# Kernel tuning notes

Measured on AMD Instinct MI355X. Metric: run time of the kernel, lower is better.

## Reference

```python
import jax, jax.numpy as jnp
import numpy as np

B, T, M, E, H = 8, 1024, 8192, 1024, 128
DECAY = 0.01
LQ_ADD = 1e-4
POS_TABLE_SIZE = 32


def setup_inputs() -> dict:
    key = jax.random.key(0)
    ks = jax.random.split(key, 9)
    return {
        "block_pos_list": jax.random.randint(ks[0], (B,), 0, 10),
        "inp": jax.random.normal(ks[1], (B, T, E), jnp.float32),
        "memory": jax.random.normal(ks[2], (B, M, E), jnp.float32),
        "memory_block_dist": jax.random.randint(ks[3], (B, M), 0, 1000).astype(jnp.int32),
        "memory_rank": jax.random.normal(ks[4], (B, M), jnp.float32),
        "pos_table": jax.random.normal(ks[5], (POS_TABLE_SIZE, E), jnp.float32) * 0.02,
        "Wk": jax.random.normal(ks[6], (H, E), jnp.float32) / np.float32(np.sqrt(E)),
        "Wq": jax.random.normal(ks[7], (H, E), jnp.float32) / np.float32(np.sqrt(E)),
        "Wv": jax.random.normal(ks[8], (H, E), jnp.float32) / np.float32(np.sqrt(E)),
    }


def reference(block_pos_list, inp, memory, memory_block_dist, memory_rank, pos_table, Wk, Wq, Wv):
    # --- reset slots where block_pos == 0 (start of a new work) ---
    reset = (block_pos_list == 0)                               # [B]
    memory = jnp.where(reset[:, None, None], 0.0, memory)       # [B, M, E]
    dist = jnp.where(reset[:, None], 0, memory_block_dist) + 1  # [B, M]

    # --- log2-bucketed positional embedding added to memory ---
    m_pos_ix = jnp.floor(jnp.log2(dist.astype(jnp.float32))).astype(jnp.int32)
    m_with_emb = memory + pos_table[m_pos_ix]                   # [B, M, E]
    mk = jnp.concatenate([m_with_emb, inp], axis=1)             # [B, M+T, E]

    # --- projections (torch Linear: x @ W.T) ---
    k = jnp.einsum('bse,he->bsh', mk, Wk)                       # [B, M+T, H]
    q = jnp.einsum('bte,he->bth', inp, Wq)                      # [B, T, H]
    v = jnp.einsum('bse,he->bsh', mk, Wv)                       # [B, M+T, H]

    # --- square + max-normalize attention (not softmax) ---
    mbs = M + T
    wei = jnp.einsum('bth,bsh->bts', q, k) * np.float32(mbs ** -0.5)  # [B, T, M+T]
    wei = wei * wei
    wei = wei / jnp.max(wei, axis=2, keepdims=True)

    # --- per-slot rank update ---
    mean_wei = jnp.mean(jnp.sum(wei, axis=1), axis=1)           # [B]
    new_rank = memory_rank + jnp.sum(wei[:, :, :M], axis=1) / mean_wei[:, None] - 1.0 - DECAY

    # --- sort memory slots by rank (descending), evict bottom block ---
    order = jnp.argsort(-new_rank, axis=1)                      # [B, M]
    mem_s = jnp.take_along_axis(memory, order[:, :, None], axis=1)
    dist_s = jnp.take_along_axis(dist, order, axis=1)
    rank_s = jnp.take_along_axis(new_rank, order, axis=1)
    r = min(T, M)
    new_memory = jax.lax.stop_gradient(mem_s.at[:, -r:].set(inp[:, -r:]))
    new_dist = dist_s.at[:, -r:].set(0)
    new_rank_out = jax.lax.stop_gradient(rank_s.at[:, -r:].set(1.0))

    qt_loss = jnp.sum(jnp.log(wei + LQ_ADD))
    out = jnp.einsum('bts,bsh->bth', wei, v)                    # [B, T, H]
    return out, qt_loss, new_memory, new_dist, new_rank_out
```

## Files before the change

### kernel.cpp

```cpp
#include <hip/hip_runtime.h>
#include <hip/hip_bf16.h>
#include <stdint.h>

#define BB 8
#define TT 1024
#define MM 8192
#define EE 1024
#define HH 128
#define SS (MM + TT)
#define RKEEP (MM - 1024)
#define NSPLIT 4
#define SCHUNK (SS / NSPLIT)
#define NT (SCHUNK / 64)
#define BK 32
#define NKVBLK (SS / 64)

typedef __attribute__((ext_vector_type(8))) short bf16x8;
typedef __attribute__((ext_vector_type(4))) short s16x4;
typedef __attribute__((ext_vector_type(4))) float f32x4;

#define SBAR()   __builtin_amdgcn_s_barrier()
#define SCB()    __builtin_amdgcn_sched_barrier(0)

static __device__ __forceinline__ unsigned f2ord(float f) {
    unsigned u = __float_as_uint(f);
    return u ^ ((u & 0x80000000u) ? 0xFFFFFFFFu : 0x80000000u);
}
static __device__ __forceinline__ float ord2f(unsigned o) {
    unsigned u = (o & 0x80000000u) ? (o ^ 0x80000000u) : ~o;
    return __uint_as_float(u);
}
static __device__ __forceinline__ unsigned short f2bf(float x) {
    unsigned u = __float_as_uint(x);
    unsigned r = u + 0x7FFFu + ((u >> 16) & 1u);
    return (unsigned short)(r >> 16);
}

static __device__ __forceinline__ void gload_lds16(const short* g, short* l) {
    __builtin_amdgcn_global_load_lds(
        (const __attribute__((address_space(1))) void*)g,
        (__attribute__((address_space(3))) void*)l, 16, 0, 0);
}

__device__ const float SCALEF = (float)(1.0 / 96.0);

__global__ __launch_bounds__(256) void k_init(
    const float* __restrict__ Wk, const float* __restrict__ Wq, const float* __restrict__ Wv,
    short* __restrict__ wk, short* __restrict__ wq, short* __restrict__ wv,
    float* __restrict__ outZ, float* __restrict__ rmax)
{
    const int blk = blockIdx.x, tid = threadIdx.x;
    if (blk < 384) {
        int idx = blk * 256 + tid;
        int m = idx >> 15;
        int o4 = (idx & 32767) * 4;
        const float* W = m == 0 ? Wk : (m == 1 ? Wq : Wv);
        short* D = m == 0 ? wk : (m == 1 ? wq : wv);
        f32x4 v = *(const f32x4*)&W[o4];
        s16x4 h;
#pragma unroll
        for (int j = 0; j < 4; ++j) h[j] = (short)f2bf(v[j]);
        *(s16x4*)&D[o4] = h;
    } else {
        const int z = (blk - 384) * 256 + tid;
        const f32x4 zero = (f32x4){0.f, 0.f, 0.f, 0.f};
        for (int i = z; i < (BB * TT * HH) / 4; i += 128 * 256)
            ((f32x4*)outZ)[i] = zero;
        if (z == 0) outZ[BB * TT * HH] = 0.f;
        if (z < (BB * TT) / 4) ((f32x4*)rmax)[z] = zero;
    }
}

__global__ __launch_bounds__(256, 3) void k_proj(
    const float* __restrict__ memory, const int* __restrict__ mbd,
    const int* __restrict__ bpl, const float* __restrict__ pos_table,
    const float* __restrict__ inp,
    const short* __restrict__ wk, const short* __restrict__ wv,
    const short* __restrict__ wq,
    short* __restrict__ kb, short* __restrict__ vT, short* __restrict__ qb)
{
    __shared__ __align__(16) short smA[2][64 * 64];
    __shared__ __align__(16) short smB[2][2][128 * 32];

    const int tid = threadIdx.x;
    const int b   = blockIdx.y;
    const int lane = tid & 63, wid = tid >> 6;
    const int wc = wid;
    const int fr = lane & 15, fq = lane >> 4;
    const int arow = tid >> 2;
    const int aq   = tid & 3;
    const int wh   = (tid >> 2);
    const int wk8  = (tid & 3) * 8;
    const int wdst = wid * 512;

    if (blockIdx.x < NKVBLK) {
        const int s0 = blockIdx.x * 64;
        const bool reset = (bpl[b] == 0);
        int pix;
        const float* abase;
        {
            int s = s0 + arow;
            if (s < MM) {
                int d = reset ? 1 : (mbd[b * MM + s] + 1);
                pix = 31 - __clz(d);
                abase = reset ? nullptr : &memory[((size_t)b * MM + s) * EE];
            } else {
                pix = -1;
                abase = &inp[((size_t)b * TT + (s - MM)) * EE];
            }
        }

        f32x4 accK[4][2], accV[4][2];
#pragma unroll
        for (int m = 0; m < 4; ++m)
#pragma unroll
            for (int n = 0; n < 2; ++n) {
                accK[m][n] = (f32x4){0.f, 0.f, 0.f, 0.f};
                accV[m][n] = (f32x4){0.f, 0.f, 0.f, 0.f};
            }

        auto STAGEW = [&](int e0, int buf) {
#pragma unroll
            for (int p = 0; p < 2; ++p) {
                int h = p * 64 + wh;
                int ec = wk8 ^ ((h & 3) << 3);
                size_t g = (size_t)h * EE + e0 + ec;
                gload_lds16(&wk[g], &smB[buf][0][p * 2048 + wdst]);
                gload_lds16(&wv[g], &smB[buf][1][p * 2048 + wdst]);
            }
        };
        auto LOADP = [&](int p, f32x4 xa[4]) {
            int e0 = p * 64 + aq * 16;
#pragma unroll
            for (int j = 0; j < 4; ++j) {
                f32x4 v = (f32x4){0.f, 0.f, 0.f, 0.f};
                if (abase) v = *(const f32x4*)&abase[e0 + j * 4];
                if (pix >= 0) {
                    f32x4 pt = *(const f32x4*)&pos_table[(size_t)pix * EE + e0 + j * 4];
                    v[0] += pt[0]; v[1] += pt[1]; v[2] += pt[2]; v[3] += pt[3];
                }
                xa[j] = v;
            }
        };
        auto STOREP = [&](const f32x4 xa[4], int abuf) {
#pragma unroll
            for (int j = 0; j < 2; ++j) {
                bf16x8 h;
#pragma unroll
                for (int c = 0; c < 4; ++c) {
                    h[c]     = (short)f2bf(xa[2 * j][c]);
                    h[4 + c] = (short)f2bf(xa[2 * j + 1][c]);
                }
                int g = (aq * 2 + j) ^ (arow & 7);
                *(bf16x8*)&smA[abuf][arow * 64 + g * 8] = h;
            }
        };

        f32x4 xa[4];
        LOADP(0, xa);
        STOREP(xa, 0);
        STAGEW(0, 0);
        __syncthreads();
        LOADP(1, xa);

        for (int step = 0; step < 32; ++step) {
            const int wbuf = step & 1;
            const int sseg = step & 1;
            const int pbuf = (step >> 1) & 1;
            if (step < 31) STAGEW((step + 1) * BK, wbuf ^ 1);

            bf16x8 ah[4];
#pragma unroll
            for (int m = 0; m < 4; ++m) {
                int r = m * 16 + fr;
                int g = (sseg * 4 + fq) ^ (r & 7);
                ah[m] = *(const bf16x8*)&smA[pbuf][r * 64 + g * 8];
            }
#pragma unroll
            for (int n = 0; n < 2; ++n) {
                int c = wc * 32 + n * 16 + fr;
                int off = c * 32 + ((fq * 8) ^ ((c & 3) << 3));
                bf16x8 kh = *(const bf16x8*)&smB[wbuf][0][off];
                bf16x8 vh = *(const bf16x8*)&smB[wbuf][1][off];
#pragma unroll
                for (int m = 0; m < 4; ++m) {
                    accK[m][n] = __builtin_amdgcn_mfma_f32_16x16x32_bf16(ah[m], kh, accK[m][n], 0, 0, 0);
                    accV[m][n] = __builtin_amdgcn_mfma_f32_16x16x32_bf16(ah[m], vh, accV[m][n], 0, 0, 0);
                }
            }
            if (sseg == 1 && step < 31) STOREP(xa, pbuf ^ 1);
            __syncthreads();
            if (sseg == 1 && step < 29) LOADP((step >> 1) + 2, xa);
        }

#pragma unroll
        for (int m = 0; m < 4; ++m) {
            int row = s0 + m * 16 + fq * 4;
#pragma unroll
            for (int n = 0; n < 2; ++n) {
                int col = wc * 32 + n * 16 + fr;
#pragma unroll
                for (int i = 0; i < 4; ++i)
                    kb[((size_t)b * SS + row + i) * HH + col] = (short)f2bf(accK[m][n][i]);
            }
        }
        float* tpT = (float*)smB;
#pragma unroll
        for (int hp = 0; hp < 4; ++hp) {
            __syncthreads();
            if (wc == hp) {
#pragma unroll
                for (int m = 0; m < 4; ++m)
#pragma unroll
                    for (int n = 0; n < 2; ++n) {
                        int cl = n * 16 + fr;
                        int row = m * 16 + fq * 4;
                        *(f32x4*)&tpT[cl * 68 + row] = accV[m][n];
                    }
            }
            __syncthreads();
            for (int idx = tid; idx < 32 * 16; idx += 256) {
                int hcl = idx >> 4, s4 = (idx & 15) << 2;
                f32x4 v = *(const f32x4*)&tpT[hcl * 68 + s4];
                s16x4 hi;
#pragma unroll
                for (int j = 0; j < 4; ++j) hi[j] = (short)f2bf(v[j]);
                size_t o = ((size_t)b * HH + hp * 32 + hcl) * SS + s0 + s4;
                *(s16x4*)&vT[o] = hi;
            }
        }
    } else {
        const int t0 = (blockIdx.x - NKVBLK) * 64;
        const float* abase = &inp[((size_t)b * TT + t0 + arow) * EE];

        f32x4 acc[4][2];
#pragma unroll
        for (int m = 0; m < 4; ++m)
#pragma unroll
            for (int n = 0; n < 2; ++n) acc[m][n] = (f32x4){0.f, 0.f, 0.f, 0.f};

        auto STAGEWQ = [&](int e0, int buf) {
#pragma unroll
            for (int p = 0; p < 2; ++p) {
                int h = p * 64 + wh;
                int ec = wk8 ^ ((h & 3) << 3);
                size_t g = (size_t)h * EE + e0 + ec;
                gload_lds16(&wq[g], &smB[buf][0][p * 2048 + wdst]);
            }
        };
        auto LOADPQ = [&](int p, f32x4 xa[4]) {
            int e0 = p * 64 + aq * 16;
#pragma unroll
            for (int j = 0; j < 4; ++j) xa[j] = *(const f32x4*)&abase[e0 + j * 4];
        };
        auto STOREPQ = [&](const f32x4 xa[4], int abuf) {
#pragma unroll
            for (int j = 0; j < 2; ++j) {
                bf16x8 h;
#pragma unroll
                for (int c = 0; c < 4; ++c) {
                    h[c]     = (short)f2bf(xa[2 * j][c]);
                    h[4 + c] = (short)f2bf(xa[2 * j + 1][c]);
                }
                int g = (aq * 2 + j) ^ (arow & 7);
                *(bf16x8*)&smA[abuf][arow * 64 + g * 8] = h;
            }
        };

        f32x4 xa[4];
        LOADPQ(0, xa);
        STOREPQ(xa, 0);
        STAGEWQ(0, 0);
        __syncthreads();
        LOADPQ(1, xa);

        for (int step = 0; step < 32; ++step) {
            const int wbuf = step & 1;
            const int sseg = step & 1;
            const int pbuf = (step >> 1) & 1;
            if (step < 31) STAGEWQ((step + 1) * BK, wbuf ^ 1);

            bf16x8 ah[4];
#pragma unroll
            for (int m = 0; m < 4; ++m) {
                int r = m * 16 + fr;
                int g = (sseg * 4 + fq) ^ (r & 7);
                ah[m] = *(const bf16x8*)&smA[pbuf][r * 64 + g * 8];
            }
#pragma unroll
            for (int n = 0; n < 2; ++n) {
                int c = wc * 32 + n * 16 + fr;
                int off = c * 32 + ((fq * 8) ^ ((c & 3) << 3));
                bf16x8 bh = *(const bf16x8*)&smB[wbuf][0][off];
#pragma unroll
                for (int m = 0; m < 4; ++m)
                    acc[m][n] = __builtin_amdgcn_mfma_f32_16x16x32_bf16(ah[m], bh, acc[m][n], 0, 0, 0);
            }
            if (sseg == 1 && step < 31) STOREPQ(xa, pbuf ^ 1);
            __syncthreads();
            if (sseg == 1 && step < 29) LOADPQ((step >> 1) + 2, xa);
        }
#pragma unroll
        for (int m = 0; m < 4; ++m) {
            int row = t0 + m * 16 + fq * 4;
#pragma unroll
            for (int n = 0; n < 2; ++n) {
                int col = wc * 32 + n * 16 + fr;
#pragma unroll
                for (int i = 0; i < 4; ++i)
                    qb[((size_t)b * TT + row + i) * HH + col] = (short)f2bf(acc[m][n][i]);
            }
        }
    }
}

__device__ __forceinline__ void stage_k64_async(const short* __restrict__ src,
                                                size_t rowBase, int tid, short* sh)
{
#pragma unroll
    for (int c2 = 0; c2 < 4; ++c2) {
        int srow = c2 * 16 + (tid >> 4);
        int scol = ((tid & 15) * 8) ^ ((srow & 7) << 3);
        size_t g = (rowBase + srow) * HH + scol;
        gload_lds16(&src[g], &sh[c2 * 2048 + (tid >> 6) * 512]);
    }
}

__device__ __forceinline__ void stage_v64_async(const short* __restrict__ vT,
                                                int b, int st, int tid, short* vs)
{
#pragma unroll
    for (int c2 = 0; c2 < 4; ++c2) {
        int h = c2 * 32 + (tid >> 3);
        int sc = ((tid & 7) * 8) ^ ((h & 7) << 3);
        size_t g = ((size_t)b * HH + h) * SS + st + sc;
        gload_lds16(&vT[g], &vs[c2 * 2048 + (tid >> 6) * 512]);
    }
}

__device__ __forceinline__ void load_qfrags(const short* __restrict__ qb,
                                            size_t rowIx, int fq, bf16x8 qh[4])
{
    size_t base = rowIx * HH + fq * 8;
#pragma unroll
    for (int k = 0; k < 4; ++k)
        qh[k] = *(const bf16x8*)&qb[base + k * 32];
}

__device__ __forceinline__ void qk_mfma4(const bf16x8 qh[4], const short* sh,
                                         int fr, int fq, f32x4 acc[4])
{
#pragma unroll
    for (int n = 0; n < 4; ++n) {
        int sc = n * 16 + fr;
        int ro = sc * 128, msk = (sc & 7) << 3;
#pragma unroll
        for (int k = 0; k < 4; ++k) {
            int off = ro + ((k * 32 + fq * 8) ^ msk);
            bf16x8 bh = *(const bf16x8*)&sh[off];
            acc[n] = __builtin_amdgcn_mfma_f32_16x16x32_bf16(qh[k], bh, acc[n], 0, 0, 0);
        }
    }
}

__device__ __forceinline__ void xcd_remap(int f, int& b, int& split, int& ttile)
{
    int xcd = f & 7, slot = f >> 3;
    int g = (slot >> 4) * 8 + xcd;
    ttile = slot & 15;
    b = g >> 2;
    split = g & 3;
}

__global__ __launch_bounds__(256) void k_rowmax(
    const short* __restrict__ qb, const short* __restrict__ kb,
    float* __restrict__ rowmax)
{
    __shared__ short Ks[2][64 * 128];
    const int tid = threadIdx.x, lane = tid & 63, wloc = tid >> 6;
    const int fr = lane & 15, fq = lane >> 4;
    int b, split, ttile;
    xcd_remap(blockIdx.x, b, split, ttile);
    const int t0 = ttile * 64;

    bf16x8 qh[4];
    load_qfrags(qb, (size_t)b * TT + t0 + wloc * 16 + fr, fq, qh);

    float rm[4] = {0.f, 0.f, 0.f, 0.f};
    const int sBeg = split * SCHUNK;
    const size_t kbase = (size_t)b * SS;

    stage_k64_async(kb, kbase + sBeg, tid, Ks[0]);
    __syncthreads();
    for (int t = 0; t < NT; ++t) {
        const int bf = t & 1;
        if (t + 1 < NT)
            stage_k64_async(kb, kbase + sBeg + (t + 1) * 64, tid, Ks[bf ^ 1]);
        f32x4 acc[4];
#pragma unroll
        for (int n = 0; n < 4; ++n) acc[n] = (f32x4){0.f, 0.f, 0.f, 0.f};
        __builtin_amdgcn_s_setprio(1);
        qk_mfma4(qh, Ks[bf], fr, fq, acc);
        __builtin_amdgcn_s_setprio(0);
#pragma unroll
        for (int n = 0; n < 4; ++n)
#pragma unroll
            for (int i = 0; i < 4; ++i) {
                float w = acc[n][i] * SCALEF;
                rm[i] = fmaxf(rm[i], w * w);
            }
        __syncthreads();
    }
#pragma unroll
    for (int d = 1; d < 16; d <<= 1)
#pragma unroll
        for (int i = 0; i < 4; ++i)
            rm[i] = fmaxf(rm[i], __shfl_xor(rm[i], d, 64));
    if (fr == 0)
#pragma unroll
        for (int i = 0; i < 4; ++i)
            atomicMax((int*)&rowmax[b * TT + t0 + wloc * 16 + fq * 4 + i], __float_as_int(rm[i]));
}

__global__ __launch_bounds__(256) void k_attn(
    const short* __restrict__ qb, const short* __restrict__ kb,
    const short* __restrict__ vT,
    const float* __restrict__ rowmax,
    float* __restrict__ outAcc, float* __restrict__ cpart, float* __restrict__ qtloss)
{
    __shared__ short Ks[2][64 * 128];
    __shared__ short Vs[2][128 * 64];
    __shared__ short Ph[64 * 64];
    __shared__ float csT[2][64];
    __shared__ float qred[256];
    const int tid = threadIdx.x, lane = tid & 63, wloc = tid >> 6;
    const int fr = lane & 15, fq = lane >> 4;
    int b, split, ttile;
    xcd_remap(blockIdx.x, b, split, ttile);
    const int t0 = ttile * 64;

    if (tid < 128) ((float*)csT)[tid] = 0.f;

    bf16x8 qh[4];
    load_qfrags(qb, (size_t)b * TT + t0 + wloc * 16 + fr, fq, qh);

    float inv[4];
#pragma unroll
    for (int i = 0; i < 4; ++i)
        inv[i] = 1.0f / rowmax[b * TT + t0 + wloc * 16 + fq * 4 + i];

    f32x4 oacc[8];
#pragma unroll
    for (int n = 0; n < 8; ++n) oacc[n] = (f32x4){0.f, 0.f, 0.f, 0.f};
    float qtp = 0.f;

    const int sBeg = split * SCHUNK;
    const size_t kbase = (size_t)b * SS;
    float* cprow = &cpart[((size_t)(b * 16 + ttile)) * SS + sBeg];

    stage_k64_async(kb, kbase + sBeg, tid, Ks[0]);
    stage_v64_async(vT, b, sBeg, tid, Vs[0]);

    for (int t = 0; t < NT; ++t) {
        const int bf = t & 1;
        __syncthreads();

        if (t + 1 < NT) {
            stage_k64_async(kb, kbase + sBeg + (t + 1) * 64, tid, Ks[bf ^ 1]);
            stage_v64_async(vT, b, sBeg + (t + 1) * 64, tid, Vs[bf ^ 1]);
        }

        f32x4 acc[4];
#pragma unroll
        for (int n = 0; n < 4; ++n) acc[n] = (f32x4){0.f, 0.f, 0.f, 0.f};
        __builtin_amdgcn_s_setprio(1);
        qk_mfma4(qh, Ks[bf], fr, fq, acc);
        __builtin_amdgcn_s_setprio(0);

        float prod = 1.f;
#pragma unroll
        for (int n = 0; n < 4; ++n) {
            float cp = 0.f;
#pragma unroll
            for (int i = 0; i < 4; ++i) {
                float w = acc[n][i] * SCALEF;
                float w2 = w * w;
                float wei = w2 * inv[i];
                prod *= (wei + 1e-4f);
                cp += wei;
                int r = wloc * 16 + fq * 4 + i;
                int sw = (n * 16 + fr) ^ ((r & 7) << 3);
                Ph[r * 64 + sw] = (short)f2bf(wei);
            }
            cp += __shfl_xor(cp, 16, 64);
            cp += __shfl_xor(cp, 32, 64);
            if (fq == 0) atomicAdd(&csT[bf][n * 16 + fr], cp);
            if (n == 1) { qtp += __logf(prod); prod = 1.f; }
        }
        qtp += __logf(prod);

        asm volatile("s_waitcnt lgkmcnt(0)" ::: "memory");
        SBAR(); SCB();
        if (tid < 64) {
            cprow[t * 64 + tid] = csT[bf][tid];
            csT[bf][tid] = 0.f;
        }
        {
            int rA = wloc * 16 + fr;
            __builtin_amdgcn_s_setprio(1);
#pragma unroll
            for (int k = 0; k < 2; ++k) {
                int offA = rA * 64 + ((k * 32 + fq * 8) ^ ((rA & 7) << 3));
                bf16x8 ph = *(const bf16x8*)&Ph[offA];
#pragma unroll
                for (int n = 0; n < 8; ++n) {
                    int hc = n * 16 + fr;
                    int offB = hc * 64 + ((k * 32 + fq * 8) ^ ((hc & 7) << 3));
                    bf16x8 vh = *(const bf16x8*)&Vs[bf][offB];
                    oacc[n] = __builtin_amdgcn_mfma_f32_16x16x32_bf16(ph, vh, oacc[n], 0, 0, 0);
                }
            }
            __builtin_amdgcn_s_setprio(0);
        }
    }

#pragma unroll
    for (int n = 0; n < 8; ++n)
#pragma unroll
        for (int i = 0; i < 4; ++i)
            atomicAdd(&outAcc[((size_t)b * TT + t0 + wloc * 16 + fq * 4 + i) * HH + n * 16 + fr],
                      oacc[n][i]);

    qred[tid] = qtp;
    __syncthreads();
    for (int off = 128; off; off >>= 1) {
        if (tid < off) qred[tid] += qred[tid + off];
        __syncthreads();
    }
    if (tid == 0) atomicAdd(qtloss, qred[0]);
}

__global__ __launch_bounds__(1024) void k_ranksort(
    const float* __restrict__ cpart, const float* __restrict__ mrank,
    float* __restrict__ csum, unsigned long long* __restrict__ keys,
    const float* __restrict__ inp, float* __restrict__ nmem,
    float* __restrict__ ndist, float* __restrict__ nrank)
{
    __shared__ unsigned long long a[MM];
    __shared__ float red[1024];
    const int blk = blockIdx.x, tid = threadIdx.x;

    if (blk >= BB) {
        const int idx = blk - BB;
        const int b = idx >> 7;
        const int r0 = RKEEP + (idx & 127) * 8;
#pragma unroll
        for (int rr = 0; rr < 2; ++rr) {
            int row = r0 + rr * 4 + (tid >> 8);
            int irow = row - RKEEP;
            int c4 = (tid & 255) * 4;
            *(f32x4*)&nmem[((size_t)b * MM + row) * EE + c4] =
                *(const f32x4*)&inp[((size_t)b * TT + irow) * EE + c4];
        }
        if (tid < 8) {
            int p = r0 + tid;
            ndist[b * MM + p] = 0.f;
            nrank[b * MM + p] = 1.0f;
        }
        return;
    }

    const int b = blk;
    float p = 0.f;
    for (int s = tid; s < SS; s += 1024) {
        float cs = 0.f;
#pragma unroll
        for (int tt = 0; tt < 16; ++tt) cs += cpart[((size_t)(b * 16 + tt)) * SS + s];
        csum[b * SS + s] = cs;
        p += cs;
    }
    red[tid] = p;
    __syncthreads();
    for (int off = 512; off; off >>= 1) {
        if (tid < off) red[tid] += red[tid + off];
        __syncthreads();
    }
    float mean = red[0] / (float)SS;
    for (int m = tid; m < MM; m += 1024) {
        float rank = ((mrank[b * MM + m] + csum[b * SS + m] / mean) - 1.0f) - 0.01f;
        a[m] = ((unsigned long long)(unsigned)(~f2ord(rank)) << 32) | (unsigned)m;
    }
    __syncthreads();

    for (int k = 2; k <= MM; k <<= 1) {
        for (int j = k >> 1; j > 0; j >>= 1) {
            for (int i = tid; i < MM; i += 1024) {
                int l = i ^ j;
                if (l > i) {
                    unsigned long long x = a[i], y = a[l];
                    bool up = ((i & k) == 0);
                    if ((x > y) == up) { a[i] = y; a[l] = x; }
                }
            }
            __syncthreads();
        }
    }
    for (int i = tid; i < MM; i += 1024) keys[(size_t)b * MM + i] = a[i];
}

__global__ __launch_bounds__(256) void k_scatter(
    const float* __restrict__ memory, const int* __restrict__ mbd,
    const int* __restrict__ bpl, const unsigned long long* __restrict__ keys,
    float* __restrict__ nmem, float* __restrict__ ndist, float* __restrict__ nrank)
{
    const int blk = blockIdx.x;
    const int b = blk / (RKEEP / 8);
    const int p0 = (blk % (RKEEP / 8)) * 8;
    const bool reset = (bpl[b] == 0);
    const int tid = threadIdx.x;
    const f32x4 zero = (f32x4){0.f, 0.f, 0.f, 0.f};

    f32x4 vr[8];
    float dist[8], rankv[8];
#pragma unroll
    for (int r = 0; r < 8; ++r) {
        int p = p0 + r;
        unsigned long long key = keys[(size_t)b * MM + p];
        int src = (int)(unsigned)(key & 0xFFFFFFFFu);
        vr[r] = reset ? zero
                      : *(const f32x4*)&memory[((size_t)b * MM + src) * EE + tid * 4];
        dist[r]  = reset ? 1.0f : (float)(mbd[b * MM + src] + 1);
        rankv[r] = ord2f(~(unsigned)(key >> 32));
    }
#pragma unroll
    for (int r = 0; r < 8; ++r) {
        int p = p0 + r;
        *(f32x4*)&nmem[((size_t)b * MM + p) * EE + tid * 4] = vr[r];
        if (tid == 0) { ndist[b * MM + p] = dist[r]; nrank[b * MM + p] = rankv[r]; }
    }
}

extern "C" void kernel_launch(void* const* d_in, const int* in_sizes, int n_in,
                              void* d_out, int out_size, void* d_ws, size_t ws_size,
                              hipStream_t stream)
{
    const int*   bpl    = (const int*)d_in[0];
    const float* inp    = (const float*)d_in[1];
    const float* memory = (const float*)d_in[2];
    const int*   mbd    = (const int*)d_in[3];
    const float* mrank  = (const float*)d_in[4];
    const float* pos    = (const float*)d_in[5];
    const float* Wk     = (const float*)d_in[6];
    const float* Wq     = (const float*)d_in[7];
    const float* Wv     = (const float*)d_in[8];

    float* out   = (float*)d_out;
    float* qtl   = out + (size_t)BB * TT * HH;
    float* nmem  = qtl + 1;
    float* ndist = nmem + (size_t)BB * MM * EE;
    float* nrank = ndist + (size_t)BB * MM;

    char* w = (char*)d_ws;
    short* qb = (short*)w; w += (size_t)BB * TT * HH * 2;
    short* kb = (short*)w; w += (size_t)BB * SS * HH * 2;
    short* vT = (short*)w; w += (size_t)BB * HH * SS * 2;
    float* rmax = (float*)w; w += (size_t)BB * TT * 4;
    float* csum = (float*)w; w += (size_t)BB * SS * 4;
    float* cpart = (float*)w; w += (size_t)BB * 16 * SS * 4;
    unsigned long long* keys = (unsigned long long*)w; w += (size_t)BB * MM * 8;
    short* wk = (short*)w; w += (size_t)HH * EE * 2;
    short* wq = (short*)w; w += (size_t)HH * EE * 2;
    short* wv = (short*)w; w += (size_t)HH * EE * 2;
    if ((size_t)(w - (char*)d_ws) > ws_size) return;

    k_init   <<<512, 256, 0, stream>>>(Wk, Wq, Wv, wk, wq, wv, out, rmax);
    k_proj   <<<dim3(NKVBLK + TT / 64, BB), 256, 0, stream>>>(memory, mbd, bpl, pos, inp,
                                                              wk, wv, wq, kb, vT, qb);
    k_rowmax <<<NSPLIT * (TT / 64) * BB, 256, 0, stream>>>(qb, kb, rmax);
    k_attn   <<<NSPLIT * (TT / 64) * BB, 256, 0, stream>>>(qb, kb, vT,
                                                           rmax, out, cpart, qtl);
    k_ranksort<<<BB + BB * 128, 1024, 0, stream>>>(cpart, mrank, csum, keys,
                                                   inp, nmem, ndist, nrank);
    k_scatter<<<BB * (RKEEP / 8), 256, 0, stream>>>(memory, mbd, bpl, keys,
                                                    nmem, ndist, nrank);
}
```

Before: 490.5 us.

## Make projection weight tiles wave-private and replace per-step block barriers with vmcnt waits

Reorganizes the weight staging in the K/V/Q projection kernel so each wave loads only the 32 head columns it consumes into its own LDS region. A wave can then wait on its own async global-to-LDS loads with explicit vmcnt counts instead of a block-wide __syncthreads every step. Block barriers remain only on odd steps, where the shared activation tile is rewritten. This removes half the barriers and lets waves drift apart, but the hand-tuned vmcnt counts must exactly match the number of outstanding loads, including the activation prefetch loads, or results may be read before they arrive.

```diff
diff --git a/kernel.cpp b/kernel.cpp
--- a/kernel.cpp
+++ b/kernel.cpp
@@ -19,6 +19,8 @@
 typedef __attribute__((ext_vector_type(4))) short s16x4;
 typedef __attribute__((ext_vector_type(4))) float f32x4;
 
+#define VMCNT(n) asm volatile("s_waitcnt vmcnt(" #n ")" ::: "memory")
+#define LGKM0()  asm volatile("s_waitcnt lgkmcnt(0)" ::: "memory")
 #define SBAR()   __builtin_amdgcn_s_barrier()
 #define SCB()    __builtin_amdgcn_sched_barrier(0)
 
@@ -80,7 +82,7 @@
     short* __restrict__ kb, short* __restrict__ vT, short* __restrict__ qb)
 {
     __shared__ __align__(16) short smA[2][64 * 64];
-    __shared__ __align__(16) short smB[2][2][128 * 32];
+    __shared__ __align__(16) short smB[2][2][4][1024];
 
     const int tid = threadIdx.x;
     const int b   = blockIdx.y;
@@ -89,9 +91,8 @@
     const int fr = lane & 15, fq = lane >> 4;
     const int arow = tid >> 2;
     const int aq   = tid & 3;
-    const int wh   = (tid >> 2);
-    const int wk8  = (tid & 3) * 8;
-    const int wdst = wid * 512;
+    const int hl0 = (lane >> 2);
+    const int sch = (lane & 3);
 
     if (blockIdx.x < NKVBLK) {
         const int s0 = blockIdx.x * 64;
@@ -121,12 +122,13 @@
 
         auto STAGEW = [&](int e0, int buf) {
 #pragma unroll
-            for (int p = 0; p < 2; ++p) {
-                int h = p * 64 + wh;
-                int ec = wk8 ^ ((h & 3) << 3);
+            for (int c2 = 0; c2 < 2; ++c2) {
+                int hlocal = c2 * 16 + hl0;
+                int h = wc * 32 + hlocal;
+                int ec = ((sch ^ (hlocal & 3)) << 3);
                 size_t g = (size_t)h * EE + e0 + ec;
-                gload_lds16(&wk[g], &smB[buf][0][p * 2048 + wdst]);
-                gload_lds16(&wv[g], &smB[buf][1][p * 2048 + wdst]);
+                gload_lds16(&wk[g], &smB[buf][0][wid][c2 * 512]);
+                gload_lds16(&wv[g], &smB[buf][1][wid][c2 * 512]);
             }
         };
         auto LOADP = [&](int p, f32x4 xa[4]) {
@@ -165,10 +167,16 @@
 
         for (int step = 0; step < 32; ++step) {
             const int wbuf = step & 1;
-            const int sseg = step & 1;
             const int pbuf = (step >> 1) & 1;
             if (step < 31) STAGEW((step + 1) * BK, wbuf ^ 1);
-
+            SCB();
+            if (step == 31)           { VMCNT(0); }
+            else if (step & 1)        { VMCNT(4); }
+            else if (step <= 28)      { VMCNT(8); }
+            else                      { VMCNT(4); }
+            SCB();
+
+            const int sseg = step & 1;
             bf16x8 ah[4];
 #pragma unroll
             for (int m = 0; m < 4; ++m) {
@@ -178,19 +186,20 @@
             }
 #pragma unroll
             for (int n = 0; n < 2; ++n) {
-                int c = wc * 32 + n * 16 + fr;
-                int off = c * 32 + ((fq * 8) ^ ((c & 3) << 3));
-                bf16x8 kh = *(const bf16x8*)&smB[wbuf][0][off];
-                bf16x8 vh = *(const bf16x8*)&smB[wbuf][1][off];
+                int off = n * 512 + fr * 32 + ((fq ^ (fr & 3)) << 3);
+                bf16x8 kh = *(const bf16x8*)&smB[wbuf][0][wid][off];
+                bf16x8 vh = *(const bf16x8*)&smB[wbuf][1][wid][off];
 #pragma unroll
                 for (int m = 0; m < 4; ++m) {
                     accK[m][n] = __builtin_amdgcn_mfma_f32_16x16x32_bf16(ah[m], kh, accK[m][n], 0, 0, 0);
                     accV[m][n] = __builtin_amdgcn_mfma_f32_16x16x32_bf16(ah[m], vh, accV[m][n], 0, 0, 0);
                 }
             }
-            if (sseg == 1 && step < 31) STOREP(xa, pbuf ^ 1);
-            __syncthreads();
-            if (sseg == 1 && step < 29) LOADP((step >> 1) + 2, xa);
+            if ((step & 1) && step < 31) {
+                STOREP(xa, pbuf ^ 1);
+                LGKM0(); SBAR(); SCB();
+                if (step < 29) LOADP((step >> 1) + 2, xa);
+            }
         }
 
 #pragma unroll
@@ -241,11 +250,12 @@
 
         auto STAGEWQ = [&](int e0, int buf) {
 #pragma unroll
-            for (int p = 0; p < 2; ++p) {
-                int h = p * 64 + wh;
-                int ec = wk8 ^ ((h & 3) << 3);
+            for (int c2 = 0; c2 < 2; ++c2) {
+                int hlocal = c2 * 16 + hl0;
+                int h = wc * 32 + hlocal;
+                int ec = ((sch ^ (hlocal & 3)) << 3);
                 size_t g = (size_t)h * EE + e0 + ec;
-                gload_lds16(&wq[g], &smB[buf][0][p * 2048 + wdst]);
+                gload_lds16(&wq[g], &smB[buf][0][wid][c2 * 512]);
             }
         };
         auto LOADPQ = [&](int p, f32x4 xa[4]) {
@@ -276,10 +286,16 @@
 
         for (int step = 0; step < 32; ++step) {
             const int wbuf = step & 1;
-            const int sseg = step & 1;
             const int pbuf = (step >> 1) & 1;
             if (step < 31) STAGEWQ((step + 1) * BK, wbuf ^ 1);
-
+            SCB();
+            if (step == 31)           { VMCNT(0); }
+            else if (step & 1)        { VMCNT(2); }
+            else if (step <= 28)      { VMCNT(6); }
+            else                      { VMCNT(2); }
+            SCB();
+
+            const int sseg = step & 1;
             bf16x8 ah[4];
 #pragma unroll
             for (int m = 0; m < 4; ++m) {
@@ -289,16 +305,17 @@
             }
 #pragma unroll
             for (int n = 0; n < 2; ++n) {
-                int c = wc * 32 + n * 16 + fr;
-                int off = c * 32 + ((fq * 8) ^ ((c & 3) << 3));
-                bf16x8 bh = *(const bf16x8*)&smB[wbuf][0][off];
+                int off = n * 512 + fr * 32 + ((fq ^ (fr & 3)) << 3);
+                bf16x8 bh = *(const bf16x8*)&smB[wbuf][0][wid][off];
 #pragma unroll
                 for (int m = 0; m < 4; ++m)
                     acc[m][n] = __builtin_amdgcn_mfma_f32_16x16x32_bf16(ah[m], bh, acc[m][n], 0, 0, 0);
             }
-            if (sseg == 1 && step < 31) STOREPQ(xa, pbuf ^ 1);
-            __syncthreads();
-            if (sseg == 1 && step < 29) LOADPQ((step >> 1) + 2, xa);
+            if ((step & 1) && step < 31) {
+                STOREPQ(xa, pbuf ^ 1);
+                LGKM0(); SBAR(); SCB();
+                if (step < 29) LOADPQ((step >> 1) + 2, xa);
+            }
         }
 #pragma unroll
         for (int m = 0; m < 4; ++m) {
@@ -499,7 +516,7 @@
         }
         qtp += __logf(prod);
 
-        asm volatile("s_waitcnt lgkmcnt(0)" ::: "memory");
+        LGKM0();
         SBAR(); SCB();
         if (tid < 64) {
             cprow[t * 64 + tid] = csT[bf][tid];
```

Measured after the change: 489.2 us. No clear change (-0.3%).
